# Performance work log

Hardware: AMD Instinct MI355X
Metric: run time of the kernel (lower is better)

Reference implementation:

```python
import jax, jax.numpy as jnp
import numpy as np

B, S, D, H = 4, 2048, 1024, 16
DK = D // H
NEG = -1000000000.0


def setup_inputs() -> dict:
    key = jax.random.key(0)
    ks = jax.random.split(key, 12)
    scale = 1.0 / np.sqrt(D)
    inp = {
        "query": jax.random.normal(ks[0], (B, S, D), jnp.float32),
        "key": jax.random.normal(ks[1], (B, S, D), jnp.float32),
        "value": jax.random.normal(ks[2], (B, S, D), jnp.float32),
        "mask": jax.random.randint(ks[3], (B, S, S), 0, 2, jnp.int32),
        "Wq": jax.random.normal(ks[4], (D, D), jnp.float32) * scale,
        "bq": jnp.zeros((D,), jnp.float32),
        "Wk": jax.random.normal(ks[5], (D, D), jnp.float32) * scale,
        "bk": jnp.zeros((D,), jnp.float32),
        "Wv": jax.random.normal(ks[6], (D, D), jnp.float32) * scale,
        "bv": jnp.zeros((D,), jnp.float32),
        "Wo": jax.random.normal(ks[7], (D, D), jnp.float32) * scale,
        "bo": jnp.zeros((D,), jnp.float32),
    }
    return inp


def _split_heads(x):
    # (B, S, D) -> (B, H, S, DK)
    return x.reshape(B, -1, H, DK).transpose(0, 2, 1, 3)


def reference(query, key, value, mask, Wq, bq, Wk, bk, Wv, bv, Wo, bo):
    q = _split_heads(query @ Wq.T + bq)
    k = _split_heads(key @ Wk.T + bk)
    v = _split_heads(value @ Wv.T + bv)
    scores = jnp.einsum('bhqd,bhkd->bhqk', q, k) / jnp.sqrt(jnp.float32(DK))
    scores = jnp.where(mask[:, None, :, :] == 0, NEG, scores)
    p_attn = jax.nn.softmax(scores, axis=-1)
    x = jnp.einsum('bhqk,bhkd->bhqd', p_attn, v)
    x = x.transpose(0, 2, 1, 3).reshape(B, -1, D)
    return x @ Wo.T + bo
```

## Files before the change

### kernel.cpp

```cpp
#include <hip/hip_runtime.h>

#define BDIM 4
#define SDIM 2048
#define DDIM 1024
#define HDIM 16
#define DKDIM 64
#define MDIM (BDIM*SDIM)

typedef __attribute__((ext_vector_type(8))) short bf16x8_t;
typedef __attribute__((ext_vector_type(4))) float f32x4_t;
typedef __attribute__((ext_vector_type(16))) float f32x16_t;

__device__ __forceinline__ unsigned short f2bf(float f) {
    union { float f; unsigned u; } v; v.f = f;
    unsigned r = v.u + 0x7FFFu + ((v.u >> 16) & 1u);
    return (unsigned short)(r >> 16);
}

__device__ __forceinline__ unsigned pkbf(float a, float b) {
    unsigned r;
    asm("v_cvt_pk_bf16_f32 %0, %1, %2" : "=v"(r) : "v"(a), "v"(b));
    return r;
}

__device__ __forceinline__ void plswap(unsigned &a, unsigned &b) {
    asm("v_permlane32_swap_b32 %0, %1" : "+v"(a), "+v"(b));
}

#if defined(__has_builtin) && __has_builtin(__builtin_amdgcn_exp2f)
#define EXP2F(x) __builtin_amdgcn_exp2f(x)
#else
#define EXP2F(x) __expf((x) * 0.69314718f)
#endif

#define QSCALE 0.18033688011112042f

__device__ __forceinline__ void gl_lds16(const void* g, void* l) {
    __builtin_amdgcn_global_load_lds(
        (const __attribute__((address_space(1))) unsigned int*)g,
        (__attribute__((address_space(3))) unsigned int*)l, 16, 0, 0);
}

__global__ void cvt3(const float* __restrict__ a, const float* __restrict__ b, const float* __restrict__ c,
                     unsigned short* __restrict__ oa, unsigned short* __restrict__ ob, unsigned short* __restrict__ oc,
                     int n4) {
    int i = blockIdx.x * blockDim.x + threadIdx.x;
    const float* s = blockIdx.y == 0 ? a : (blockIdx.y == 1 ? b : c);
    unsigned short* d = blockIdx.y == 0 ? oa : (blockIdx.y == 1 ? ob : oc);
    if (i < n4) {
        float4 v = ((const float4*)s)[i];
        uint2 o;
        o.x = pkbf(v.x, v.y);
        o.y = pkbf(v.z, v.w);
        ((uint2*)d)[i] = o;
    }
}

__global__ void cvt4(const float* __restrict__ a, const float* __restrict__ b,
                     const float* __restrict__ c, const float* __restrict__ e,
                     unsigned short* __restrict__ oa, unsigned short* __restrict__ ob,
                     unsigned short* __restrict__ oc, unsigned short* __restrict__ oe,
                     int n4) {
    int i = blockIdx.x * blockDim.x + threadIdx.x;
    const float* s = blockIdx.y == 0 ? a : (blockIdx.y == 1 ? b : (blockIdx.y == 2 ? c : e));
    unsigned short* d = blockIdx.y == 0 ? oa : (blockIdx.y == 1 ? ob : (blockIdx.y == 2 ? oc : oe));
    if (i < n4) {
        float4 v = ((const float4*)s)[i];
        uint2 o;
        o.x = pkbf(v.x, v.y);
        o.y = pkbf(v.z, v.w);
        ((uint2*)d)[i] = o;
    }
}

__global__ void pack_mask(const int* __restrict__ m, unsigned long long* __restrict__ bits) {
    int g = blockIdx.x * 256 + threadIdx.x;
    unsigned long long bal = __ballot(m[g] != 0);
    if ((threadIdx.x & 63) == 0) bits[g >> 6] = bal;
}

__global__ __launch_bounds__(256) void gemm_qkv(
    const unsigned short* __restrict__ A0, const unsigned short* __restrict__ A1,
    const unsigned short* __restrict__ A2,
    const unsigned short* __restrict__ B0, const unsigned short* __restrict__ B1,
    const unsigned short* __restrict__ B2,
    const float* __restrict__ bi0, const float* __restrict__ bi1, const float* __restrict__ bi2,
    unsigned short* __restrict__ C0, unsigned short* __restrict__ C1,
    unsigned short* __restrict__ C2)
{
    __shared__ unsigned short As[2][128 * 32];
    __shared__ unsigned short Bs[2][128 * 32];
    const int K = DDIM, M = MDIM, N = DDIM;
    const int z = blockIdx.z;
    const unsigned short* A = z == 0 ? A0 : (z == 1 ? A1 : A2);
    const unsigned short* Bw = z == 0 ? B0 : (z == 1 ? B1 : B2);
    const float* bias = z == 0 ? bi0 : (z == 1 ? bi1 : bi2);
    unsigned short* Cb = z == 0 ? C0 : (z == 1 ? C1 : C2);
    const float scale = z == 0 ? QSCALE : 1.0f;

    const int tid = threadIdx.x;
    const int w = tid >> 6, lane = tid & 63;
    const int wr = w >> 1, wc = w & 1;
    const int quad = lane >> 4, l16 = lane & 15;
    const int bn = blockIdx.x, bm = blockIdx.y;

    const int rl = lane >> 2;
    const int cl = (((lane & 3) ^ ((rl >> 1) & 3)) * 8);
    const int sw = (l16 >> 1) & 3;
    const int c0 = w * 2;
    const unsigned short* gA = A + (size_t)(bm * 128 + c0 * 16 + rl) * K + cl;
    const unsigned short* gB = Bw + (size_t)(bn * 128 + c0 * 16 + rl) * K + cl;
    const int ldsoff = c0 * 512 + lane * 8;

    f32x4_t acc[4][4] = {};

    gl_lds16(gA, &As[0][ldsoff]);
    gl_lds16(gA + (size_t)16 * K, &As[0][ldsoff + 16 * 32]);
    gl_lds16(gB, &Bs[0][ldsoff]);
    gl_lds16(gB + (size_t)16 * K, &Bs[0][ldsoff + 16 * 32]);

    int cur = 0;
    for (int k0 = 0; k0 < K; k0 += 32) {
        __syncthreads();
        if (k0 + 32 < K) {
            const unsigned short* nA = gA + k0 + 32;
            const unsigned short* nB = gB + k0 + 32;
            gl_lds16(nA, &As[cur ^ 1][ldsoff]);
            gl_lds16(nA + (size_t)16 * K, &As[cur ^ 1][ldsoff + 16 * 32]);
            gl_lds16(nB, &Bs[cur ^ 1][ldsoff]);
            gl_lds16(nB + (size_t)16 * K, &Bs[cur ^ 1][ldsoff + 16 * 32]);
        }
        bf16x8_t af[4], bfr[4];
#pragma unroll
        for (int mi = 0; mi < 4; ++mi)
            af[mi] = *(const bf16x8_t*)(&As[cur][(wr * 64 + mi * 16 + l16) * 32 + (quad ^ sw) * 8]);
#pragma unroll
        for (int ni = 0; ni < 4; ++ni)
            bfr[ni] = *(const bf16x8_t*)(&Bs[cur][(wc * 64 + ni * 16 + l16) * 32 + (quad ^ sw) * 8]);
#pragma unroll
        for (int mi = 0; mi < 4; ++mi)
#pragma unroll
            for (int ni = 0; ni < 4; ++ni)
                acc[mi][ni] = __builtin_amdgcn_mfma_f32_16x16x32_bf16(af[mi], bfr[ni], acc[mi][ni], 0, 0, 0);
        cur ^= 1;
    }

#pragma unroll
    for (int mi = 0; mi < 4; ++mi) {
#pragma unroll
        for (int ni = 0; ni < 4; ++ni) {
            const int n = bn * 128 + wc * 64 + ni * 16 + l16;
            const int m0 = bm * 128 + wr * 64 + mi * 16 + quad * 4;
            const float bv = bias[n];
            if (z == 2) {
                uint2 pk2;
                pk2.x = pkbf(acc[mi][ni][0] + bv, acc[mi][ni][1] + bv);
                pk2.y = pkbf(acc[mi][ni][2] + bv, acc[mi][ni][3] + bv);
                *(uint2*)(Cb + (size_t)n * M + m0) = pk2;
            } else {
                unsigned pa = pkbf((acc[mi][ni][0] + bv) * scale, (acc[mi][ni][1] + bv) * scale);
                unsigned pb = pkbf((acc[mi][ni][2] + bv) * scale, (acc[mi][ni][3] + bv) * scale);
                Cb[(size_t)(m0 + 0) * N + n] = (unsigned short)pa;
                Cb[(size_t)(m0 + 1) * N + n] = (unsigned short)(pa >> 16);
                Cb[(size_t)(m0 + 2) * N + n] = (unsigned short)pb;
                Cb[(size_t)(m0 + 3) * N + n] = (unsigned short)(pb >> 16);
            }
        }
    }
}

__global__ __launch_bounds__(256) void gemm_out(
    const unsigned short* __restrict__ A,
    const unsigned short* __restrict__ Bw,
    const float* __restrict__ bias,
    float* __restrict__ Cf)
{
    __shared__ unsigned short As[2][128 * 32];
    __shared__ unsigned short Bs[2][128 * 32];
    const int K = DDIM, N = DDIM;
    const int tid = threadIdx.x;
    const int w = tid >> 6, lane = tid & 63;
    const int wr = w >> 1, wc = w & 1;
    const int quad = lane >> 4, l16 = lane & 15;
    const int bn = blockIdx.x, bm = blockIdx.y;

    const int rl = lane >> 2;
    const int cl = (((lane & 3) ^ ((rl >> 1) & 3)) * 8);
    const int sw = (l16 >> 1) & 3;
    const int c0 = w * 2;
    const unsigned short* gA = A + (size_t)(bm * 128 + c0 * 16 + rl) * K + cl;
    const unsigned short* gB = Bw + (size_t)(bn * 128 + c0 * 16 + rl) * K + cl;
    const int ldsoff = c0 * 512 + lane * 8;

    f32x4_t acc[4][4] = {};

    gl_lds16(gA, &As[0][ldsoff]);
    gl_lds16(gA + (size_t)16 * K, &As[0][ldsoff + 16 * 32]);
    gl_lds16(gB, &Bs[0][ldsoff]);
    gl_lds16(gB + (size_t)16 * K, &Bs[0][ldsoff + 16 * 32]);

    int cur = 0;
    for (int k0 = 0; k0 < K; k0 += 32) {
        __syncthreads();
        if (k0 + 32 < K) {
            const unsigned short* nA = gA + k0 + 32;
            const unsigned short* nB = gB + k0 + 32;
            gl_lds16(nA, &As[cur ^ 1][ldsoff]);
            gl_lds16(nA + (size_t)16 * K, &As[cur ^ 1][ldsoff + 16 * 32]);
            gl_lds16(nB, &Bs[cur ^ 1][ldsoff]);
            gl_lds16(nB + (size_t)16 * K, &Bs[cur ^ 1][ldsoff + 16 * 32]);
        }
        bf16x8_t af[4], bfr[4];
#pragma unroll
        for (int mi = 0; mi < 4; ++mi)
            af[mi] = *(const bf16x8_t*)(&As[cur][(wr * 64 + mi * 16 + l16) * 32 + (quad ^ sw) * 8]);
#pragma unroll
        for (int ni = 0; ni < 4; ++ni)
            bfr[ni] = *(const bf16x8_t*)(&Bs[cur][(wc * 64 + ni * 16 + l16) * 32 + (quad ^ sw) * 8]);
#pragma unroll
        for (int mi = 0; mi < 4; ++mi)
#pragma unroll
            for (int ni = 0; ni < 4; ++ni)
                acc[mi][ni] = __builtin_amdgcn_mfma_f32_16x16x32_bf16(af[mi], bfr[ni], acc[mi][ni], 0, 0, 0);
        cur ^= 1;
    }

#pragma unroll
    for (int mi = 0; mi < 4; ++mi) {
#pragma unroll
        for (int ni = 0; ni < 4; ++ni) {
            const int n = bn * 128 + wc * 64 + ni * 16 + l16;
            const int m0 = bm * 128 + wr * 64 + mi * 16 + quad * 4;
            const float bv = bias[n];
#pragma unroll
            for (int r = 0; r < 4; ++r)
                Cf[(size_t)(m0 + r) * N + n] = acc[mi][ni][r] + bv;
        }
    }
}

__global__ __launch_bounds__(256, 4) void attn_kernel(
    const unsigned short* __restrict__ Qp,
    const unsigned short* __restrict__ Kp,
    const unsigned short* __restrict__ Vt,
    const unsigned long long* __restrict__ mbits,
    unsigned short* __restrict__ Xa)
{
    __shared__ unsigned short SMEM[16384];
    const int tid = threadIdx.x, w = tid >> 6, lane = tid & 63;
    const int l32 = lane & 31, hi = lane >> 5;
    const int bx = blockIdx.x;
    const int h = bx & 15, qt = (bx >> 4) & 15, b = bx >> 8;
    const int q0 = qt * 128;
    const int rl = lane >> 2;
    const int cl = (((lane & 3) ^ ((rl >> 1) & 3)) * 8);
    const int swl = (l32 >> 1) & 3;
    const int lbase = (l32 >> 4) * 512 + (l32 & 15) * 32 + ((hi ^ swl) * 8);
    const int myq = b * SDIM + q0 + w * 32 + l32;

    bf16x8_t qf[4];
    {
        const unsigned short* gq = Qp + (size_t)myq * DDIM + h * 64 + hi * 8;
#pragma unroll
        for (int c = 0; c < 4; ++c)
            qf[c] = *(const bf16x8_t*)(gq + c * 16);
    }

    const unsigned long long* mq = mbits + (size_t)myq * 32;

    const int cc0 = w * 2, cc1 = w * 2 + 1;
    const unsigned short* gK0 = Kp + (size_t)(b * SDIM + (cc0 & 3) * 16 + rl) * DDIM + h * 64 + (cc0 >> 2) * 32 + cl;
    const unsigned short* gK1 = Kp + (size_t)(b * SDIM + (cc1 & 3) * 16 + rl) * DDIM + h * 64 + (cc1 >> 2) * 32 + cl;
    const unsigned short* gV0 = Vt + (size_t)(h * 64 + (cc0 & 3) * 16 + rl) * MDIM + b * SDIM + (cc0 >> 2) * 32 + cl;
    const unsigned short* gV1 = Vt + (size_t)(h * 64 + (cc1 & 3) * 16 + rl) * MDIM + b * SDIM + (cc1 >> 2) * 32 + cl;
    unsigned short* dK0 = SMEM + cc0 * 512 + lane * 8;
    unsigned short* dK1 = SMEM + cc1 * 512 + lane * 8;
    unsigned short* dV0 = SMEM + 8192 + cc0 * 512 + lane * 8;
    unsigned short* dV1 = SMEM + 8192 + cc1 * 512 + lane * 8;

    gl_lds16(gK0, dK0);
    gl_lds16(gK1, dK1);
    gl_lds16(gV0, dV0);
    gl_lds16(gV1, dV1);
    unsigned long long nm = mq[0];

    f32x16_t o0 = {}, o1 = {}, o4 = {};
    union { unsigned u[4]; bf16x8_t v; } ones;
    ones.u[0] = ones.u[1] = ones.u[2] = ones.u[3] = 0x3F803F80u;

    int cur = 0;
    for (int kt = 0; kt < SDIM / 64; ++kt) {
        __syncthreads();
        const unsigned long long mysh = nm >> (4 * hi);
        const unsigned mw0 = (unsigned)mysh;
        const unsigned mw1 = (unsigned)(mysh >> 32);

        if (kt + 1 < SDIM / 64) {
            const int nb = (cur ^ 1) * 4096;
            const size_t ko = (size_t)(kt + 1) * 64 * DDIM;
            const size_t vo = (size_t)(kt + 1) * 64;
            gl_lds16(gK0 + ko, dK0 + nb);
            gl_lds16(gK1 + ko, dK1 + nb);
            gl_lds16(gV0 + vo, dV0 + nb);
            gl_lds16(gV1 + vo, dV1 + nb);
            nm = mq[kt + 1];
        }
        const unsigned short* Ksb = SMEM + cur * 4096;
        const unsigned short* Vsb = SMEM + 8192 + cur * 4096;

#pragma unroll
        for (int t = 0; t < 2; ++t) {
            f32x16_t s = {};
#pragma unroll
            for (int c = 0; c < 4; ++c) {
                const bf16x8_t ak = *(const bf16x8_t*)(Ksb + (c >> 1) * 2048 + t * 1024 + (lbase ^ ((c & 1) * 16)));
                s = __builtin_amdgcn_mfma_f32_32x32x16_bf16(ak, qf[c], s, 0, 0, 0);
            }
            const unsigned wm = t ? mw1 : mw0;
            float p[16];
#pragma unroll
            for (int r = 0; r < 16; ++r) {
                const int pos = (r & 3) + 8 * (r >> 2);
                const float pe = EXP2F(s[r]);
                const int mm = (int)(wm << (31 - pos)) >> 31;
                p[r] = __uint_as_float(__float_as_uint(pe) & (unsigned)mm);
            }
#pragma unroll
            for (int c2 = 0; c2 < 2; ++c2) {
                unsigned d0 = pkbf(p[c2 * 8 + 0], p[c2 * 8 + 1]);
                unsigned d1 = pkbf(p[c2 * 8 + 2], p[c2 * 8 + 3]);
                unsigned d2 = pkbf(p[c2 * 8 + 4], p[c2 * 8 + 5]);
                unsigned d3 = pkbf(p[c2 * 8 + 6], p[c2 * 8 + 7]);
                plswap(d0, d2);
                plswap(d1, d3);
                union { unsigned u[4]; bf16x8_t v; } pf;
                pf.u[0] = d0; pf.u[1] = d1; pf.u[2] = d2; pf.u[3] = d3;
                const bf16x8_t va0 = *(const bf16x8_t*)(Vsb + t * 2048 + (lbase ^ (c2 * 16)));
                const bf16x8_t va1 = *(const bf16x8_t*)(Vsb + t * 2048 + 1024 + (lbase ^ (c2 * 16)));
                o0 = __builtin_amdgcn_mfma_f32_32x32x16_bf16(va0, pf.v, o0, 0, 0, 0);
                o1 = __builtin_amdgcn_mfma_f32_32x32x16_bf16(va1, pf.v, o1, 0, 0, 0);
                o4 = __builtin_amdgcn_mfma_f32_32x32x16_bf16(ones.v, pf.v, o4, 0, 0, 0);
            }
        }
        cur ^= 1;
    }

    __syncthreads();
    unsigned short* T = SMEM + w * 2304;
    const float rcp = 1.0f / o4[0];
#pragma unroll
    for (int pi = 0; pi < 8; ++pi) {
        const int dk = (pi & 1) * 2 + 8 * (pi >> 1) + 4 * hi;
        *(unsigned*)&T[l32 * 72 + dk]      = pkbf(o0[2 * pi] * rcp, o0[2 * pi + 1] * rcp);
        *(unsigned*)&T[l32 * 72 + 32 + dk] = pkbf(o1[2 * pi] * rcp, o1[2 * pi + 1] * rcp);
    }
    const int rrow = lane >> 1;
    const unsigned short* Trow = SMEM + w * 2304 + rrow * 72 + (lane & 1) * 32;
    unsigned short* dst = Xa + (size_t)(b * SDIM + q0 + w * 32 + rrow) * DDIM + h * 64 + (lane & 1) * 32;
#pragma unroll
    for (int i = 0; i < 4; ++i)
        *(bf16x8_t*)(dst + i * 8) = *(const bf16x8_t*)(Trow + i * 8);
}

extern "C" void kernel_launch(void* const* d_in, const int* in_sizes, int n_in,
                              void* d_out, int out_size, void* d_ws, size_t ws_size,
                              hipStream_t stream)
{
    const float* query = (const float*)d_in[0];
    const float* key   = (const float*)d_in[1];
    const float* value = (const float*)d_in[2];
    const int*   mask  = (const int*)d_in[3];
    const float* Wq = (const float*)d_in[4];  const float* bq = (const float*)d_in[5];
    const float* Wk = (const float*)d_in[6];  const float* bk = (const float*)d_in[7];
    const float* Wv = (const float*)d_in[8];  const float* bv = (const float*)d_in[9];
    const float* Wo = (const float*)d_in[10]; const float* bo = (const float*)d_in[11];

    const size_t MD = (size_t)MDIM * DDIM;
    const size_t DD = (size_t)DDIM * DDIM;

    unsigned short* qb  = (unsigned short*)d_ws;
    unsigned short* kb  = qb + MD;
    unsigned short* vb  = kb + MD;
    unsigned short* wqb = vb + MD;
    unsigned short* wkb = wqb + DD;
    unsigned short* wvb = wkb + DD;
    unsigned short* wob = wvb + DD;
    unsigned short* Qp  = wob + DD;
    unsigned short* Kp  = Qp + MD;
    unsigned short* Vt  = Kp + MD;
    unsigned short* Xa  = Vt + MD;
    unsigned long long* mbits = (unsigned long long*)qb;

    {
        const int n4m = (int)(MD / 4), n4d = (int)(DD / 4);
        dim3 g3((n4m + 255) / 256, 3), g4((n4d + 255) / 256, 4);
        cvt3<<<g3, 256, 0, stream>>>(query, key, value, qb, kb, vb, n4m);
        cvt4<<<g4, 256, 0, stream>>>(Wq, Wk, Wv, Wo, wqb, wkb, wvb, wob, n4d);
    }

    dim3 gq(DDIM / 128, MDIM / 128, 3);
    gemm_qkv<<<gq, 256, 0, stream>>>(qb, kb, vb, wqb, wkb, wvb, bq, bk, bv, Qp, Kp, Vt);

    pack_mask<<<(BDIM * SDIM * SDIM) / 256, 256, 0, stream>>>(mask, mbits);

    attn_kernel<<<BDIM * HDIM * (SDIM / 128), 256, 0, stream>>>(Qp, Kp, Vt, mbits, Xa);

    dim3 gg(DDIM / 128, MDIM / 128);
    gemm_out<<<gg, 256, 0, stream>>>(Xa, wob, bo, (float*)d_out);
}
```

Before: 419.5 us.

## Swizzle block IDs per XCD, transpose MFMA operands for vector stores, add setprio

```diff
diff --git a/kernel.cpp b/kernel.cpp
--- a/kernel.cpp
+++ b/kernel.cpp
@@ -31,6 +31,12 @@
 #define EXP2F(x) __builtin_amdgcn_exp2f(x)
 #else
 #define EXP2F(x) __expf((x) * 0.69314718f)
+#endif
+
+#if defined(__has_builtin) && __has_builtin(__builtin_amdgcn_sbfe)
+#define SBFE1(x, p) __builtin_amdgcn_sbfe((int)(x), (p), 1)
+#else
+#define SBFE1(x, p) (((int)((x) << (31 - (p)))) >> 31)
 #endif
 
 #define QSCALE 0.18033688011112042f
@@ -91,7 +97,12 @@
     __shared__ unsigned short As[2][128 * 32];
     __shared__ unsigned short Bs[2][128 * 32];
     const int K = DDIM, M = MDIM, N = DDIM;
-    const int z = blockIdx.z;
+    const int bid = blockIdx.x;
+    const int swz = (bid & 7) * 192 + (bid >> 3);
+    const int z = swz >> 9;
+    const int rem = swz & 511;
+    const int bm = rem >> 3, bn = rem & 7;
+
     const unsigned short* A = z == 0 ? A0 : (z == 1 ? A1 : A2);
     const unsigned short* Bw = z == 0 ? B0 : (z == 1 ? B1 : B2);
     const float* bias = z == 0 ? bi0 : (z == 1 ? bi1 : bi2);
@@ -102,7 +113,6 @@
     const int w = tid >> 6, lane = tid & 63;
     const int wr = w >> 1, wc = w & 1;
     const int quad = lane >> 4, l16 = lane & 15;
-    const int bn = blockIdx.x, bm = blockIdx.y;
 
     const int rl = lane >> 2;
     const int cl = (((lane & 3) ^ ((rl >> 1) & 3)) * 8);
@@ -137,33 +147,48 @@
 #pragma unroll
         for (int ni = 0; ni < 4; ++ni)
             bfr[ni] = *(const bf16x8_t*)(&Bs[cur][(wc * 64 + ni * 16 + l16) * 32 + (quad ^ sw) * 8]);
-#pragma unroll
-        for (int mi = 0; mi < 4; ++mi)
-#pragma unroll
-            for (int ni = 0; ni < 4; ++ni)
-                acc[mi][ni] = __builtin_amdgcn_mfma_f32_16x16x32_bf16(af[mi], bfr[ni], acc[mi][ni], 0, 0, 0);
+        if (z == 2) {
+#pragma unroll
+            for (int mi = 0; mi < 4; ++mi)
+#pragma unroll
+                for (int ni = 0; ni < 4; ++ni)
+                    acc[mi][ni] = __builtin_amdgcn_mfma_f32_16x16x32_bf16(af[mi], bfr[ni], acc[mi][ni], 0, 0, 0);
+        } else {
+#pragma unroll
+            for (int mi = 0; mi < 4; ++mi)
+#pragma unroll
+                for (int ni = 0; ni < 4; ++ni)
+                    acc[mi][ni] = __builtin_amdgcn_mfma_f32_16x16x32_bf16(bfr[ni], af[mi], acc[mi][ni], 0, 0, 0);
+        }
         cur ^= 1;
     }
 
-#pragma unroll
-    for (int mi = 0; mi < 4; ++mi) {
-#pragma unroll
-        for (int ni = 0; ni < 4; ++ni) {
-            const int n = bn * 128 + wc * 64 + ni * 16 + l16;
-            const int m0 = bm * 128 + wr * 64 + mi * 16 + quad * 4;
-            const float bv = bias[n];
-            if (z == 2) {
+    if (z == 2) {
+#pragma unroll
+        for (int mi = 0; mi < 4; ++mi) {
+#pragma unroll
+            for (int ni = 0; ni < 4; ++ni) {
+                const int n = bn * 128 + wc * 64 + ni * 16 + l16;
+                const int m0 = bm * 128 + wr * 64 + mi * 16 + quad * 4;
+                const float bv = bias[n];
                 uint2 pk2;
                 pk2.x = pkbf(acc[mi][ni][0] + bv, acc[mi][ni][1] + bv);
                 pk2.y = pkbf(acc[mi][ni][2] + bv, acc[mi][ni][3] + bv);
                 *(uint2*)(Cb + (size_t)n * M + m0) = pk2;
-            } else {
-                unsigned pa = pkbf((acc[mi][ni][0] + bv) * scale, (acc[mi][ni][1] + bv) * scale);
-                unsigned pb = pkbf((acc[mi][ni][2] + bv) * scale, (acc[mi][ni][3] + bv) * scale);
-                Cb[(size_t)(m0 + 0) * N + n] = (unsigned short)pa;
-                Cb[(size_t)(m0 + 1) * N + n] = (unsigned short)(pa >> 16);
-                Cb[(size_t)(m0 + 2) * N + n] = (unsigned short)pb;
-                Cb[(size_t)(m0 + 3) * N + n] = (unsigned short)(pb >> 16);
+            }
+        }
+    } else {
+#pragma unroll
+        for (int mi = 0; mi < 4; ++mi) {
+#pragma unroll
+            for (int ni = 0; ni < 4; ++ni) {
+                const int n0 = bn * 128 + wc * 64 + ni * 16 + quad * 4;
+                const int m = bm * 128 + wr * 64 + mi * 16 + l16;
+                const float4 bv4 = *(const float4*)&bias[n0];
+                uint2 pk2;
+                pk2.x = pkbf((acc[mi][ni][0] + bv4.x) * scale, (acc[mi][ni][1] + bv4.y) * scale);
+                pk2.y = pkbf((acc[mi][ni][2] + bv4.z) * scale, (acc[mi][ni][3] + bv4.w) * scale);
+                *(uint2*)(Cb + (size_t)m * N + n0) = pk2;
             }
         }
     }
@@ -178,11 +203,13 @@
     __shared__ unsigned short As[2][128 * 32];
     __shared__ unsigned short Bs[2][128 * 32];
     const int K = DDIM, N = DDIM;
+    const int bid = blockIdx.x;
+    const int swz = (bid & 7) * 64 + (bid >> 3);
+    const int bm = swz >> 3, bn = swz & 7;
     const int tid = threadIdx.x;
     const int w = tid >> 6, lane = tid & 63;
     const int wr = w >> 1, wc = w & 1;
     const int quad = lane >> 4, l16 = lane & 15;
-    const int bn = blockIdx.x, bm = blockIdx.y;
 
     const int rl = lane >> 2;
     const int cl = (((lane & 3) ^ ((rl >> 1) & 3)) * 8);
@@ -221,7 +248,7 @@
         for (int mi = 0; mi < 4; ++mi)
 #pragma unroll
             for (int ni = 0; ni < 4; ++ni)
-                acc[mi][ni] = __builtin_amdgcn_mfma_f32_16x16x32_bf16(af[mi], bfr[ni], acc[mi][ni], 0, 0, 0);
+                acc[mi][ni] = __builtin_amdgcn_mfma_f32_16x16x32_bf16(bfr[ni], af[mi], acc[mi][ni], 0, 0, 0);
         cur ^= 1;
     }
 
@@ -229,12 +256,15 @@
     for (int mi = 0; mi < 4; ++mi) {
 #pragma unroll
         for (int ni = 0; ni < 4; ++ni) {
-            const int n = bn * 128 + wc * 64 + ni * 16 + l16;
-            const int m0 = bm * 128 + wr * 64 + mi * 16 + quad * 4;
-            const float bv = bias[n];
-#pragma unroll
-            for (int r = 0; r < 4; ++r)
-                Cf[(size_t)(m0 + r) * N + n] = acc[mi][ni][r] + bv;
+            const int n0 = bn * 128 + wc * 64 + ni * 16 + quad * 4;
+            const int m = bm * 128 + wr * 64 + mi * 16 + l16;
+            const float4 bv4 = *(const float4*)&bias[n0];
+            float4 o;
+            o.x = acc[mi][ni][0] + bv4.x;
+            o.y = acc[mi][ni][1] + bv4.y;
+            o.z = acc[mi][ni][2] + bv4.z;
+            o.w = acc[mi][ni][3] + bv4.w;
+            *(float4*)(Cf + (size_t)m * N + n0) = o;
         }
     }
 }
@@ -249,8 +279,9 @@
     __shared__ unsigned short SMEM[16384];
     const int tid = threadIdx.x, w = tid >> 6, lane = tid & 63;
     const int l32 = lane & 31, hi = lane >> 5;
-    const int bx = blockIdx.x;
-    const int h = bx & 15, qt = (bx >> 4) & 15, b = bx >> 8;
+    const int bid = blockIdx.x;
+    const int swz = (bid & 7) * 128 + (bid >> 3);
+    const int qt = swz & 15, h = (swz >> 4) & 15, b = swz >> 8;
     const int q0 = qt * 128;
     const int rl = lane >> 2;
     const int cl = (((lane & 3) ^ ((rl >> 1) & 3)) * 8);
@@ -311,18 +342,20 @@
 #pragma unroll
         for (int t = 0; t < 2; ++t) {
             f32x16_t s = {};
+            __builtin_amdgcn_s_setprio(1);
 #pragma unroll
             for (int c = 0; c < 4; ++c) {
                 const bf16x8_t ak = *(const bf16x8_t*)(Ksb + (c >> 1) * 2048 + t * 1024 + (lbase ^ ((c & 1) * 16)));
                 s = __builtin_amdgcn_mfma_f32_32x32x16_bf16(ak, qf[c], s, 0, 0, 0);
             }
+            __builtin_amdgcn_s_setprio(0);
             const unsigned wm = t ? mw1 : mw0;
             float p[16];
 #pragma unroll
             for (int r = 0; r < 16; ++r) {
                 const int pos = (r & 3) + 8 * (r >> 2);
                 const float pe = EXP2F(s[r]);
-                const int mm = (int)(wm << (31 - pos)) >> 31;
+                const int mm = SBFE1(wm, pos);
                 p[r] = __uint_as_float(__float_as_uint(pe) & (unsigned)mm);
             }
 #pragma unroll
@@ -337,9 +370,11 @@
                 pf.u[0] = d0; pf.u[1] = d1; pf.u[2] = d2; pf.u[3] = d3;
                 const bf16x8_t va0 = *(const bf16x8_t*)(Vsb + t * 2048 + (lbase ^ (c2 * 16)));
                 const bf16x8_t va1 = *(const bf16x8_t*)(Vsb + t * 2048 + 1024 + (lbase ^ (c2 * 16)));
+                __builtin_amdgcn_s_setprio(1);
                 o0 = __builtin_amdgcn_mfma_f32_32x32x16_bf16(va0, pf.v, o0, 0, 0, 0);
                 o1 = __builtin_amdgcn_mfma_f32_32x32x16_bf16(va1, pf.v, o1, 0, 0, 0);
                 o4 = __builtin_amdgcn_mfma_f32_32x32x16_bf16(ones.v, pf.v, o4, 0, 0, 0);
+                __builtin_amdgcn_s_setprio(0);
             }
         }
         cur ^= 1;
@@ -398,13 +433,11 @@
         cvt4<<<g4, 256, 0, stream>>>(Wq, Wk, Wv, Wo, wqb, wkb, wvb, wob, n4d);
     }
 
-    dim3 gq(DDIM / 128, MDIM / 128, 3);
-    gemm_qkv<<<gq, 256, 0, stream>>>(qb, kb, vb, wqb, wkb, wvb, bq, bk, bv, Qp, Kp, Vt);
+    gemm_qkv<<<1536, 256, 0, stream>>>(qb, kb, vb, wqb, wkb, wvb, bq, bk, bv, Qp, Kp, Vt);
 
     pack_mask<<<(BDIM * SDIM * SDIM) / 256, 256, 0, stream>>>(mask, mbits);
 
     attn_kernel<<<BDIM * HDIM * (SDIM / 128), 256, 0, stream>>>(Qp, Kp, Vt, mbits, Xa);
 
-    dim3 gg(DDIM / 128, MDIM / 128);
-    gemm_out<<<gg, 256, 0, stream>>>(Xa, wob, bo, (float*)d_out);
-}
+    gemm_out<<<512, 256, 0, stream>>>(Xa, wob, bo, (float*)d_out);
+}
```

Measured after the change: 482.2 us. 1.15x slower.
